# Kernel tuning notes

Measured on AMD Instinct MI355X. Metric: run time of the kernel, lower is better.

## Reference

```python
import jax, jax.numpy as jnp
import numpy as np

N = 4_000_000   # number of rows
F = 32          # num_feature
P = 100_000     # number of segments (p)


def setup_inputs() -> dict:
    key = jax.random.key(0)
    k1, k2, k3, k4 = jax.random.split(key, 4)
    feats = jax.random.normal(k1, (N, F), dtype=jnp.float32)
    # nn.Linear(num_feature, 1): weight [1, F], bias [1]
    W = jax.random.normal(k2, (1, F), dtype=jnp.float32) / np.sqrt(F)
    b = jax.random.normal(k3, (1,), dtype=jnp.float32) * 0.01
    idx = jax.random.randint(k4, (N,), 0, P, dtype=jnp.int64)
    return {"feats": feats, "W": W, "b": b, "idx": idx, "p": P}


def reference(feats, W, b, idx, p):
    # per-row linear projection to a scalar: r[n] = feats[n] . W[0] + b[0]
    r = jnp.einsum("nf,f->n", feats, W[0]) + b[0]
    # c starts at zeros and is updated when r >= c[t]  =>  c = max(0, segment_max(r))
    seg = jax.ops.segment_max(r, idx, num_segments=p)  # empty segments -> -inf
    return jnp.maximum(seg, 0.0)
```

## Files before the change

### kernel.cpp

```cpp
#include <hip/hip_runtime.h>


__global__ __launch_bounds__(256) void miniNN_seglinmax_kernel(
    const float4* __restrict__ feats4,
    const float*  __restrict__ W,
    const float*  __restrict__ b,
    const int*    __restrict__ idx,
    int*          __restrict__ out_i,
    int           n_rows)
{
    const int lane            = threadIdx.x & 63;
    const int sub             = lane & 7;
    const int waves_per_block = blockDim.x >> 6;
    const long long gwid   = (long long)blockIdx.x * waves_per_block + (threadIdx.x >> 6);
    const long long nwaves = (long long)gridDim.x * waves_per_block;

    const float4 wv  = ((const float4*)W)[sub];
    const float bias = b[0];

    const long long ngroups = n_rows >> 3;
    for (long long g = gwid; g < ngroups; g += nwaves) {
        const long long base4 = g << 6;
        const float4 v = feats4[base4 + lane];
        float s = v.x * wv.x + v.y * wv.y + v.z * wv.z + v.w * wv.w;
        s += __shfl_xor(s, 1);
        s += __shfl_xor(s, 2);
        s += __shfl_xor(s, 4);
        if (sub == 0) {
            const long long row = (g << 3) + (lane >> 3);
            const float r = s + bias;
            if (r > 0.0f) {
                atomicMax(&out_i[idx[row]], __float_as_int(r));
            }
        }
    }

    const long long tail_start = ngroups << 3;
    const long long gtid = (long long)blockIdx.x * blockDim.x + threadIdx.x;
    const long long row  = tail_start + gtid;
    if (row < n_rows) {
        const float* f = (const float*)feats4 + row * 32;
        float r = bias;
        #pragma unroll
        for (int k = 0; k < 32; ++k) r += f[k] * W[k];
        if (r > 0.0f) {
            atomicMax(&out_i[idx[row]], __float_as_int(r));
        }
    }
}

extern "C" void kernel_launch(void* const* d_in, const int* in_sizes, int n_in,
                              void* d_out, int out_size, void* d_ws, size_t ws_size,
                              hipStream_t stream) {
    const float* feats = (const float*)d_in[0];
    const float* W     = (const float*)d_in[1];
    const float* b     = (const float*)d_in[2];
    const int*   idx   = (const int*)d_in[3];
    const int n_rows   = in_sizes[0] / 32;

    hipMemsetAsync(d_out, 0, (size_t)out_size * sizeof(float), stream);

    const int threads = 256;
    const int blocks  = 2048;
    miniNN_seglinmax_kernel<<<blocks, threads, 0, stream>>>(
        (const float4*)feats, W, b, idx, (int*)d_out, n_rows);
}
```

Measured before the change: 125.4 us.

## Process 32 rows per wave iteration with batched loads and tail-balanced grid

```diff
diff --git a/kernel.cpp b/kernel.cpp
--- a/kernel.cpp
+++ b/kernel.cpp
@@ -1,4 +1,5 @@
 #include <hip/hip_runtime.h>
+#include <limits.h>
 
 
 __global__ __launch_bounds__(256) void miniNN_seglinmax_kernel(
@@ -9,43 +10,59 @@
     int*          __restrict__ out_i,
     int           n_rows)
 {
-    const int lane            = threadIdx.x & 63;
-    const int sub             = lane & 7;
-    const int waves_per_block = blockDim.x >> 6;
-    const long long gwid   = (long long)blockIdx.x * waves_per_block + (threadIdx.x >> 6);
-    const long long nwaves = (long long)gridDim.x * waves_per_block;
+    const int lane = threadIdx.x & 63;
+    const int sub  = lane & 7;
+    const int j    = lane >> 3;
+    const int gwid = blockIdx.x * (blockDim.x >> 6) + (threadIdx.x >> 6);
+    const int nw   = gridDim.x * (blockDim.x >> 6);
 
     const float4 wv  = ((const float4*)W)[sub];
     const float bias = b[0];
 
-    const long long ngroups = n_rows >> 3;
-    for (long long g = gwid; g < ngroups; g += nwaves) {
-        const long long base4 = g << 6;
-        const float4 v = feats4[base4 + lane];
-        float s = v.x * wv.x + v.y * wv.y + v.z * wv.z + v.w * wv.w;
-        s += __shfl_xor(s, 1);
-        s += __shfl_xor(s, 2);
-        s += __shfl_xor(s, 4);
+    const int nsuper = n_rows >> 5;
+    for (int sg = gwid; sg < nsuper; sg += nw) {
+        const float4* p = feats4 + (sg << 8) + lane;
+        const float4 v0 = p[0];
+        const float4 v1 = p[64];
+        const float4 v2 = p[128];
+        const float4 v3 = p[192];
+
+        float s0 = v0.x * wv.x + v0.y * wv.y + v0.z * wv.z + v0.w * wv.w;
+        float s1 = v1.x * wv.x + v1.y * wv.y + v1.z * wv.z + v1.w * wv.w;
+        float s2 = v2.x * wv.x + v2.y * wv.y + v2.z * wv.z + v2.w * wv.w;
+        float s3 = v3.x * wv.x + v3.y * wv.y + v3.z * wv.z + v3.w * wv.w;
+
+        s0 += __shfl_xor(s0, 1); s0 += __shfl_xor(s0, 2); s0 += __shfl_xor(s0, 4);
+        s1 += __shfl_xor(s1, 1); s1 += __shfl_xor(s1, 2); s1 += __shfl_xor(s1, 4);
+        s2 += __shfl_xor(s2, 1); s2 += __shfl_xor(s2, 2); s2 += __shfl_xor(s2, 4);
+        s3 += __shfl_xor(s3, 1); s3 += __shfl_xor(s3, 2); s3 += __shfl_xor(s3, 4);
+
         if (sub == 0) {
-            const long long row = (g << 3) + (lane >> 3);
-            const float r = s + bias;
-            if (r > 0.0f) {
-                atomicMax(&out_i[idx[row]], __float_as_int(r));
-            }
+            const int rowbase = (sg << 5) + j;
+            const int i0 = idx[rowbase];
+            const int i1 = idx[rowbase + 8];
+            const int i2 = idx[rowbase + 16];
+            const int i3 = idx[rowbase + 24];
+            const float r0 = s0 + bias;
+            const float r1 = s1 + bias;
+            const float r2 = s2 + bias;
+            const float r3 = s3 + bias;
+            if (r0 > 0.0f) atomicMax(out_i + i0, __float_as_int(r0));
+            if (r1 > 0.0f) atomicMax(out_i + i1, __float_as_int(r1));
+            if (r2 > 0.0f) atomicMax(out_i + i2, __float_as_int(r2));
+            if (r3 > 0.0f) atomicMax(out_i + i3, __float_as_int(r3));
         }
     }
 
-    const long long tail_start = ngroups << 3;
-    const long long gtid = (long long)blockIdx.x * blockDim.x + threadIdx.x;
-    const long long row  = tail_start + gtid;
+    const int tail_start = nsuper << 5;
+    const int gtid = blockIdx.x * blockDim.x + threadIdx.x;
+    const int row  = tail_start + gtid;
     if (row < n_rows) {
-        const float* f = (const float*)feats4 + row * 32;
+        const float* f = (const float*)feats4 + (long long)row * 32;
         float r = bias;
         #pragma unroll
         for (int k = 0; k < 32; ++k) r += f[k] * W[k];
-        if (r > 0.0f) {
-            atomicMax(&out_i[idx[row]], __float_as_int(r));
-        }
+        if (r > 0.0f) atomicMax(out_i + idx[row], __float_as_int(r));
     }
 }
 
@@ -60,8 +77,16 @@
 
     hipMemsetAsync(d_out, 0, (size_t)out_size * sizeof(float), stream);
 
-    const int threads = 256;
-    const int blocks  = 2048;
-    miniNN_seglinmax_kernel<<<blocks, threads, 0, stream>>>(
+    const int nsuper = n_rows >> 5;
+    int best_blocks = 2048;
+    long best_waste = LONG_MAX;
+    for (int blk = 1024; blk <= 4096; ++blk) {
+        const long waves = (long)blk * 4;
+        const long iters = (nsuper + waves - 1) / waves;
+        const long waste = iters * waves - nsuper;
+        if (waste < best_waste) { best_waste = waste; best_blocks = blk; }
+    }
+
+    miniNN_seglinmax_kernel<<<best_blocks, 256, 0, stream>>>(
         (const float4*)feats, W, b, idx, (int*)d_out, n_rows);
 }
```

Measured after the change: 119.2 us. 4.9% less time.
